# Kernel optimization log

Hardware: AMD Instinct MI355X
Metric: run time of the kernel (lower is better)

Reference implementation:

```python
import jax, jax.numpy as jnp
import numpy as np
from jax import lax

DIM, HEADS, HIDDEN = 384, 6, 1536
B, D, H, W = 2, 14, 14, 14
LN_EPS = 1e-5


def setup_inputs() -> dict:
    key = jax.random.key(0)
    ks = jax.random.split(key, 8)
    s = 0.02
    return {
        "x": jax.random.normal(ks[0], (B, DIM, D, H, W), jnp.float32),
        "conv_w": jax.random.normal(ks[1], (DIM, 1, 3, 3, 3), jnp.float32) * s,
        "conv_b": jnp.zeros((DIM,), jnp.float32),
        "ln1_w": jnp.ones((DIM,), jnp.float32),
        "ln1_b": jnp.zeros((DIM,), jnp.float32),
        "qkv_w": jax.random.normal(ks[2], (3 * DIM, DIM), jnp.float32) * s,
        "proj_w": jax.random.normal(ks[3], (DIM, DIM), jnp.float32) * s,
        "proj_b": jnp.zeros((DIM,), jnp.float32),
        "ln2_w": jnp.ones((DIM,), jnp.float32),
        "ln2_b": jnp.zeros((DIM,), jnp.float32),
        "fc1_w": jax.random.normal(ks[4], (HIDDEN, DIM), jnp.float32) * s,
        "fc1_b": jnp.zeros((HIDDEN,), jnp.float32),
        "fc2_w": jax.random.normal(ks[5], (DIM, HIDDEN), jnp.float32) * s,
        "fc2_b": jnp.zeros((DIM,), jnp.float32),
    }


def _layernorm(x, w, b):
    mu = jnp.mean(x, axis=-1, keepdims=True)
    var = jnp.var(x, axis=-1, keepdims=True)
    return (x - mu) * lax.rsqrt(var + LN_EPS) * w + b


def reference(x, conv_w, conv_b, ln1_w, ln1_b, qkv_w, proj_w, proj_b,
              ln2_w, ln2_b, fc1_w, fc1_b, fc2_w, fc2_b):
    Bn, C = x.shape[0], x.shape[1]
    Dd, Hh, Ww = x.shape[2], x.shape[3], x.shape[4]
    # depthwise conv3d positional embedding (groups=dim), padding=1
    pos = lax.conv_general_dilated(
        x, conv_w, window_strides=(1, 1, 1), padding="SAME",
        feature_group_count=C,
        dimension_numbers=("NCDHW", "OIDHW", "NCDHW"))
    x = x + pos + conv_b[None, :, None, None, None] * 0 + conv_b[None, :, None, None, None]
    # fix: bias belongs to conv output only once
    x = x - conv_b[None, :, None, None, None]
    N = Dd * Hh * Ww
    t = x.reshape(Bn, C, N).transpose(0, 2, 1)  # [B, N, C]

    # attention
    hd = C // HEADS
    scale = hd ** -0.5
    tn = _layernorm(t, ln1_w, ln1_b)
    qkv = tn @ qkv_w.T  # [B, N, 3C]
    qkv = qkv.reshape(Bn, N, 3, HEADS, hd).transpose(2, 0, 3, 1, 4)
    q, k, v = qkv[0], qkv[1], qkv[2]  # [B, H, N, hd]
    attn = jax.nn.softmax(jnp.einsum("bhnd,bhmd->bhnm", q, k) * scale, axis=-1)
    o = jnp.einsum("bhnm,bhmd->bhnd", attn, v)
    o = o.transpose(0, 2, 1, 3).reshape(Bn, N, C)
    t = t + o @ proj_w.T + proj_b

    # MLP (exact GELU, matching torch nn.GELU default)
    tn2 = _layernorm(t, ln2_w, ln2_b)
    h = jax.nn.gelu(tn2 @ fc1_w.T + fc1_b, approximate=False)
    t = t + h @ fc2_w.T + fc2_b

    return t.transpose(0, 2, 1).reshape(Bn, C, Dd, Hh, Ww)
```

## Files before the change

### kernel.cpp

```cpp
#include <hip/hip_runtime.h>
#include <hip/hip_bf16.h>
#include <math.h>

#define DIM 384
#define HEADS 6
#define HIDDEN 1536
#define NTOK 2744
#define NTOKP 2752
#define BATCH 2
#define MTOT (BATCH * NTOK)
#define KSPLIT 4
#define NQT 11
#define CEXP 0.18033688f

typedef __bf16 bf16x8 __attribute__((ext_vector_type(8)));
typedef __bf16 bf16x4 __attribute__((ext_vector_type(4)));
typedef float  f32x4  __attribute__((ext_vector_type(4)));

#define F_GELU  1
#define F_RESID 2
#define F_BF16  4
#define F_QKV   8
#define F_TRANS 16

__device__ __forceinline__ void gll16(const void* g, void* l) {
    __builtin_amdgcn_global_load_lds(
        (const __attribute__((address_space(1))) unsigned int*)g,
        (__attribute__((address_space(3))) unsigned int*)l, 16, 0, 0);
}

__global__ void k_conv(const float* __restrict__ x, const float* __restrict__ cw,
                       float* __restrict__ t,
                       const float* __restrict__ w0, const float* __restrict__ w1,
                       const float* __restrict__ w2, const float* __restrict__ w3,
                       __bf16* o0, __bf16* o1, __bf16* o2, __bf16* o3,
                       __bf16* vt_pad) {
    int bid = blockIdx.x;
    if (bid >= 2256) {
        #pragma unroll
        for (int k = 0; k < 6; k++) {
            int idx = k * 256 + threadIdx.x;
            int row = idx >> 1, half = idx & 1;
            bf16x4 z4 = { (__bf16)0.f, (__bf16)0.f, (__bf16)0.f, (__bf16)0.f };
            *(bf16x4*)(vt_pad + (size_t)row * NTOKP + 2732 + half * 16) = z4;
        }
        return;
    }
    if (bid >= 528) {
        int i = (bid - 528) * 256 + threadIdx.x;
        const float* s; __bf16* d; int off;
        if (i < 110592)      { s = w0; d = o0; off = i; }
        else if (i < 147456) { s = w1; d = o1; off = i - 110592; }
        else if (i < 294912) { s = w2; d = o2; off = i - 147456; }
        else                 { s = w3; d = o3; off = i - 294912; }
        float4 v = ((const float4*)s)[off];
        bf16x4 bb = { (__bf16)v.x, (__bf16)v.y, (__bf16)v.z, (__bf16)v.w };
        *(bf16x4*)(d + (size_t)off * 4) = bb;
        return;
    }
    int nb = bid % 11, rest = bid / 11;
    int cb = rest % 24, b = rest / 24;
    int c0 = cb * 16;
    int n = nb * 256 + threadIdx.x;
    if (n >= NTOK) return;
    int d = n / 196, r = n % 196, h = r / 14, w = r % 14;
    const float* xb = x + ((size_t)b * DIM + c0) * NTOK;
    float acc[16];
    #pragma unroll
    for (int c = 0; c < 16; c++) acc[c] = xb[(size_t)c * NTOK + n];
    #pragma unroll
    for (int kd = 0; kd < 3; kd++) {
        int dd = d + kd - 1;
        if (dd < 0 || dd >= 14) continue;
        #pragma unroll
        for (int kh = 0; kh < 3; kh++) {
            int hh = h + kh - 1;
            if (hh < 0 || hh >= 14) continue;
            #pragma unroll
            for (int kw = 0; kw < 3; kw++) {
                int ww = w + kw - 1;
                if (ww < 0 || ww >= 14) continue;
                int np = (dd * 14 + hh) * 14 + ww;
                int tap = kd * 9 + kh * 3 + kw;
                #pragma unroll
                for (int c = 0; c < 16; c++)
                    acc[c] = fmaf(cw[(c0 + c) * 27 + tap], xb[(size_t)c * NTOK + np], acc[c]);
            }
        }
    }
    float* tp = t + (size_t)(b * NTOK + n) * DIM + c0;
    #pragma unroll
    for (int c = 0; c < 16; c += 4) {
        float4 v = { acc[c], acc[c + 1], acc[c + 2], acc[c + 3] };
        *(float4*)(tp + c) = v;
    }
}

__device__ __forceinline__ void ln_body(const float* __restrict__ in,
                                        __bf16* __restrict__ out,
                                        const float* __restrict__ w,
                                        const float* __restrict__ b) {
    int wid = threadIdx.x >> 6, lane = threadIdx.x & 63;
    int token = blockIdx.x * 4 + wid;
    const float* row = in + (size_t)token * DIM;
    float v[6], s = 0.f, s2 = 0.f;
    #pragma unroll
    for (int i = 0; i < 6; i++) {
        v[i] = row[lane + 64 * i];
        s += v[i]; s2 += v[i] * v[i];
    }
    #pragma unroll
    for (int m = 1; m < 64; m <<= 1) { s += __shfl_xor(s, m); s2 += __shfl_xor(s2, m); }
    float mu = s * (1.f / DIM);
    float rstd = rsqrtf(s2 * (1.f / DIM) - mu * mu + 1e-5f);
    __bf16* orow = out + (size_t)token * DIM;
    #pragma unroll
    for (int i = 0; i < 6; i++) {
        int c = lane + 64 * i;
        orow[c] = (__bf16)((v[i] - mu) * rstd * w[c] + b[c]);
    }
}
__global__ void k_ln1(const float* in, __bf16* out, const float* w, const float* b) {
    ln_body(in, out, w, b);
}
__global__ void k_ln2(const float* in, __bf16* out, const float* w, const float* b) {
    ln_body(in, out, w, b);
}

__device__ __forceinline__ void gemm12864_body(
    const __bf16* __restrict__ A, const __bf16* __restrict__ B,
    const float* __restrict__ bias, void* __restrict__ out,
    __bf16* __restrict__ vt_out, int M, int N, int K, int flags) {
    __shared__ __bf16 As[128][64];
    __shared__ __bf16 Bs[64][64];
    int tid = threadIdx.x, lane = tid & 63, wid = tid >> 6;
    int quad = lane >> 4, l16 = lane & 15;
    int wm = wid & 1, wn = wid >> 1;
    int m0 = blockIdx.y * 128, n0 = blockIdx.x * 64;
    int x7 = l16 & 7;

    auto stage = [&](int k0) {
        #pragma unroll
        for (int i = 0; i < 4; i++) {
            int c = i * 256 + tid;
            int row = c >> 3, cc = (c & 7) ^ (row & 7);
            int gm = m0 + row; if (gm > M - 1) gm = M - 1;
            gll16(A + (size_t)gm * K + k0 + cc * 8, &As[0][0] + (size_t)c * 8);
        }
        #pragma unroll
        for (int i = 0; i < 2; i++) {
            int c = i * 256 + tid;
            int row = c >> 3, cc = (c & 7) ^ (row & 7);
            gll16(B + (size_t)(n0 + row) * K + k0 + cc * 8, &Bs[0][0] + (size_t)c * 8);
        }
    };

    f32x4 acc[4][2] = {};
    int nk = K >> 6;
    for (int ki = 0; ki < nk; ki++) {
        if (ki) __syncthreads();
        stage(ki << 6);
        __syncthreads();
        #pragma unroll
        for (int s = 0; s < 2; s++) {
            bf16x8 a[4], b[2];
            #pragma unroll
            for (int i = 0; i < 4; i++)
                a[i] = *(bf16x8*)&As[wm * 64 + i * 16 + l16][(((s * 4 + quad) ^ x7)) * 8];
            #pragma unroll
            for (int j = 0; j < 2; j++)
                b[j] = *(bf16x8*)&Bs[wn * 32 + j * 16 + l16][(((s * 4 + quad) ^ x7)) * 8];
            #pragma unroll
            for (int i = 0; i < 4; i++)
                #pragma unroll
                for (int j = 0; j < 2; j++)
                    acc[i][j] = __builtin_amdgcn_mfma_f32_16x16x32_bf16(a[i], b[j], acc[i][j], 0, 0, 0);
        }
    }

    int colb = n0 + wn * 32;
    #pragma unroll
    for (int j = 0; j < 2; j++) {
        int col = colb + j * 16 + l16;
        float bv = bias ? bias[col] : 0.f;
        #pragma unroll
        for (int i = 0; i < 4; i++) {
            int row0 = m0 + wm * 64 + i * 16 + quad * 4;
            if (row0 >= M) continue;
            float v4[4];
            #pragma unroll
            for (int r = 0; r < 4; r++) {
                float v = acc[i][j][r] + bv;
                if (flags & F_GELU) v = 0.5f * v * (1.f + erff(v * 0.70710678f));
                if ((flags & F_QKV) && col < 384) v *= CEXP;
                v4[r] = v;
            }
            if ((flags & F_QKV) && col >= 768) {
                int b2 = row0 / NTOK, n2 = row0 - b2 * NTOK;
                int n2p = (n2 & ~63) | (((n2 >> 2) & 3) << 4) | (((n2 >> 4) & 3) << 2);
                bf16x4 pk = { (__bf16)v4[0], (__bf16)v4[1], (__bf16)v4[2], (__bf16)v4[3] };
                *(bf16x4*)(vt_out + ((size_t)(b2 * DIM + (col - 768))) * NTOKP + n2p) = pk;
            } else {
                #pragma unroll
                for (int r = 0; r < 4; r++)
                    ((__bf16*)out)[(size_t)(row0 + r) * N + col] = (__bf16)v4[r];
            }
        }
    }
}
__global__ __launch_bounds__(256) void k_qkv(const __bf16* A, const __bf16* B,
        void* out, __bf16* vt_out, int M, int N, int K) {
    gemm12864_body(A, B, nullptr, out, vt_out, M, N, K, F_QKV);
}
__global__ __launch_bounds__(256) void k_fc1(const __bf16* A, const __bf16* B,
        const float* bias, void* out, int M, int N, int K) {
    gemm12864_body(A, B, bias, out, nullptr, M, N, K, F_GELU | F_BF16);
}

__device__ __forceinline__ void gemm64_body(
    const __bf16* __restrict__ A, const __bf16* __restrict__ B,
    const float* __restrict__ bias, const float* __restrict__ resid,
    void* __restrict__ out, int M, int N, int K, int flags) {
    __shared__ __align__(16) char sm[17408];
    __bf16 (*As)[64] = (__bf16(*)[64])sm;
    __bf16 (*Bs)[64] = (__bf16(*)[64])(sm + 8192);
    float* Tt = (float*)sm;
    int tid = threadIdx.x, lane = tid & 63, wid = tid >> 6;
    int quad = lane >> 4, l16 = lane & 15;
    int wm = wid & 1, wn = wid >> 1;
    int m0 = blockIdx.y * 64, n0 = blockIdx.x * 64;
    int x7 = l16 & 7;

    auto stage = [&](int k0) {
        #pragma unroll
        for (int i = 0; i < 2; i++) {
            int c = i * 256 + tid;
            int row = c >> 3, cc = (c & 7) ^ (row & 7);
            int gm = m0 + row; if (gm > M - 1) gm = M - 1;
            gll16(A + (size_t)gm * K + k0 + cc * 8, &As[0][0] + (size_t)c * 8);
        }
        #pragma unroll
        for (int i = 0; i < 2; i++) {
            int c = i * 256 + tid;
            int row = c >> 3, cc = (c & 7) ^ (row & 7);
            gll16(B + (size_t)(n0 + row) * K + k0 + cc * 8, &Bs[0][0] + (size_t)c * 8);
        }
    };

    f32x4 acc[2][2] = {};
    int nk = K >> 6;
    for (int ki = 0; ki < nk; ki++) {
        if (ki) __syncthreads();
        stage(ki << 6);
        __syncthreads();
        #pragma unroll
        for (int s = 0; s < 2; s++) {
            bf16x8 a[2], b[2];
            #pragma unroll
            for (int i = 0; i < 2; i++)
                a[i] = *(bf16x8*)&As[wm * 32 + i * 16 + l16][(((s * 4 + quad) ^ x7)) * 8];
            #pragma unroll
            for (int j = 0; j < 2; j++)
                b[j] = *(bf16x8*)&Bs[wn * 32 + j * 16 + l16][(((s * 4 + quad) ^ x7)) * 8];
            #pragma unroll
            for (int i = 0; i < 2; i++)
                #pragma unroll
                for (int j = 0; j < 2; j++)
                    acc[i][j] = __builtin_amdgcn_mfma_f32_16x16x32_bf16(a[i], b[j], acc[i][j], 0, 0, 0);
        }
    }

    if (flags & F_TRANS) {
        #pragma unroll
        for (int half = 0; half < 2; half++) {
            __syncthreads();
            if (wn == half) {
                #pragma unroll
                for (int j = 0; j < 2; j++) {
                    int colL = j * 16 + l16;
                    int col = n0 + half * 32 + colL;
                    float bv = bias[col];
                    #pragma unroll
                    for (int i = 0; i < 2; i++) {
                        int rowL = wm * 32 + i * 16 + quad * 4;
                        float v4[4];
                        #pragma unroll
                        for (int r = 0; r < 4; r++) {
                            int rr = m0 + rowL + r; if (rr > M - 1) rr = M - 1;
                            v4[r] = acc[i][j][r] + bv + resid[(size_t)rr * N + col];
                        }
                        float4 pk = { v4[0], v4[1], v4[2], v4[3] };
                        *(float4*)&Tt[colL * 68 + rowL] = pk;
                    }
                }
            }
            __syncthreads();
            int c = tid >> 3, no = (tid & 7) * 8;
            int col = n0 + half * 32 + c;
            #pragma unroll
            for (int q2 = 0; q2 < 2; q2++) {
                int nn = no + q2 * 4;
                int row = m0 + nn;
                if (row >= M) continue;
                int b2 = row / NTOK, n2 = row - b2 * NTOK;
                float4 v = *(float4*)&Tt[c * 68 + nn];
                *(float4*)((float*)out + ((size_t)(b2 * N + col)) * NTOK + n2) = v;
            }
        }
        return;
    }

    #pragma unroll
    for (int j = 0; j < 2; j++) {
        int col = n0 + wn * 32 + j * 16 + l16;
        float bv = bias ? bias[col] : 0.f;
        #pragma unroll
        for (int i = 0; i < 2; i++) {
            int row0 = m0 + wm * 32 + i * 16 + quad * 4;
            if (row0 >= M) continue;
            #pragma unroll
            for (int r = 0; r < 4; r++) {
                float v = acc[i][j][r] + bv;
                if (flags & F_RESID) v += resid[(size_t)(row0 + r) * N + col];
                ((float*)out)[(size_t)(row0 + r) * N + col] = v;
            }
        }
    }
}
__global__ __launch_bounds__(256) void k_proj(const __bf16* A, const __bf16* B,
        const float* bias, const float* resid, void* out, int M, int N, int K) {
    gemm64_body(A, B, bias, resid, out, M, N, K, F_RESID);
}
__global__ __launch_bounds__(256) void k_fc2(const __bf16* A, const __bf16* B,
        const float* bias, const float* resid, void* out, int M, int N, int K) {
    gemm64_body(A, B, bias, resid, out, M, N, K, F_RESID | F_TRANS);
}

__global__ __launch_bounds__(512, 4) void k_attn(const __bf16* __restrict__ qkv,
                                                 const __bf16* __restrict__ vt,
                                                 __bf16* __restrict__ opart,
                                                 float* __restrict__ lpart) {
    __shared__ __align__(16) __bf16 KV[2][2][64][64];
    __bf16 (*Qs)[64] = (__bf16(*)[64])KV;

    int tid = threadIdx.x, lane = tid & 63, wid = tid >> 6;
    int quad = lane >> 4, l16 = lane & 15;
    int flat = blockIdx.x;
    int xcd = flat & 7, slot = flat >> 3;
    int grp = slot / 11, qb = slot - grp * 11;
    int g = xcd + 8 * grp;
    int bh = g % 12, ks = g / 12;
    int q0 = qb * 256;
    int b = bh / HEADS, h = bh % HEADS;
    int x7 = l16 & 7;

    int kt0 = (43 * ks) / KSPLIT, kt1 = (43 * (ks + 1)) / KSPLIT;

    int srow = tid >> 3, scc = (tid & 7) ^ (srow & 7);
    const __bf16* pK = qkv + ((size_t)(b * NTOK + kt0 * 64 + srow)) * 1152 + 384 + h * 64 + scc * 8;
    const __bf16* pV = vt + ((size_t)(bh * 64 + srow)) * NTOKP + kt0 * 64 + scc * 8;

    auto stageKV = [&](int kt, int bufi) {
        const __bf16* kp = pK + (size_t)(kt - kt0) * (64 * 1152);
        if (kt == 42 && srow >= 56)
            kp = qkv + ((size_t)(b * NTOK + NTOK - 1)) * 1152 + 384 + h * 64 + scc * 8;
        gll16(kp, &KV[bufi][0][0][0] + (size_t)tid * 8);
        gll16(pV + (size_t)(kt - kt0) * 64, &KV[bufi][1][0][0] + (size_t)tid * 8);
    };

    #pragma unroll
    for (int i = 0; i < 4; i++) {
        int c = i * 512 + tid;
        int row = c >> 3, cc = (c & 7) ^ (row & 7);
        int gq = q0 + row; if (gq > NTOK - 1) gq = NTOK - 1;
        gll16(qkv + ((size_t)(b * NTOK + gq)) * 1152 + h * 64 + cc * 8,
              &Qs[0][0] + (size_t)c * 8);
    }
    __syncthreads();

    bf16x8 aq[2][2];
    #pragma unroll
    for (int qt = 0; qt < 2; qt++)
        #pragma unroll
        for (int sx = 0; sx < 2; sx++)
            aq[qt][sx] = *(bf16x8*)&Qs[wid * 32 + qt * 16 + l16][((sx * 4 + quad) ^ x7) * 8];
    __syncthreads();

    stageKV(kt0, 0);

    int koff0 = (quad ^ x7) * 8, koff1 = ((4 + quad) ^ x7) * 8;
    int voff0 = ((quad * 2 + 0) ^ x7) * 8, voff1 = ((quad * 2 + 1) ^ x7) * 8;

    const f32x4 fzero = {0.f, 0.f, 0.f, 0.f};
    f32x4 oaccT[2][4] = {};
    float l_sum[2] = {0.f, 0.f};

    int bufi = 0;
    for (int kt = kt0; kt < kt1; kt++) {
        __syncthreads();
        if (kt + 1 < kt1) stageKV(kt + 1, bufi ^ 1);

        const __bf16* ksb = &KV[bufi][0][0][0] + l16 * 64;
        const __bf16* vtb = &KV[bufi][1][0][0] + l16 * 64;
        bool tail = (kt == 42);

        bf16x8 pb[2][2];
        #pragma unroll
        for (int t = 0; t < 4; t++) {
            bf16x8 bk0 = *(bf16x8*)(ksb + t * 1024 + koff0);
            bf16x8 bk1 = *(bf16x8*)(ksb + t * 1024 + koff1);
            #pragma unroll
            for (int qt = 0; qt < 2; qt++) {
                f32x4 z = __builtin_amdgcn_mfma_f32_16x16x32_bf16(bk0, aq[qt][0], fzero, 0, 0, 0);
                z = __builtin_amdgcn_mfma_f32_16x16x32_bf16(bk1, aq[qt][1], z, 0, 0, 0);
                float e0 = exp2f(z[0]), e1 = exp2f(z[1]), e2 = exp2f(z[2]), e3 = exp2f(z[3]);
                if (tail) {
                    int kb = kt * 64 + t * 16 + quad * 4;
                    if (kb + 0 >= NTOK) e0 = 0.f;
                    if (kb + 1 >= NTOK) e1 = 0.f;
                    if (kb + 2 >= NTOK) e2 = 0.f;
                    if (kb + 3 >= NTOK) e3 = 0.f;
                }
                l_sum[qt] += (e0 + e1) + (e2 + e3);
                int half = (t & 1) * 4, px = t >> 1;
                pb[qt][px][half + 0] = (__bf16)e0;
                pb[qt][px][half + 1] = (__bf16)e1;
                pb[qt][px][half + 2] = (__bf16)e2;
                pb[qt][px][half + 3] = (__bf16)e3;
            }
        }

        #pragma unroll
        for (int dt = 0; dt < 4; dt++) {
            const __bf16* vr = vtb + dt * 1024;
            bf16x8 av0 = *(bf16x8*)(vr + voff0);
            bf16x8 av1 = *(bf16x8*)(vr + voff1);
            #pragma unroll
            for (int qt = 0; qt < 2; qt++) {
                oaccT[qt][dt] = __builtin_amdgcn_mfma_f32_16x16x32_bf16(av0, pb[qt][0], oaccT[qt][dt], 0, 0, 0);
                oaccT[qt][dt] = __builtin_amdgcn_mfma_f32_16x16x32_bf16(av1, pb[qt][1], oaccT[qt][dt], 0, 0, 0);
            }
        }
        bufi ^= 1;
    }

    #pragma unroll
    for (int qt = 0; qt < 2; qt++) {
        float l = l_sum[qt];
        l += __shfl_xor(l, 16);
        l += __shfl_xor(l, 32);
        int gq = q0 + wid * 32 + qt * 16 + l16;
        if (quad == 0 && gq < NTOK)
            lpart[((size_t)ks * 12 + bh) * NTOK + gq] = l;
    }

    __bf16* op = opart + ((((size_t)(ks * 12 + bh) * 11 + qb) * 8 + wid) * 2048);
    #pragma unroll
    for (int qt = 0; qt < 2; qt++)
        #pragma unroll
        for (int dt = 0; dt < 4; dt++) {
            bf16x4 pk = { (__bf16)oaccT[qt][dt][0], (__bf16)oaccT[qt][dt][1],
                          (__bf16)oaccT[qt][dt][2], (__bf16)oaccT[qt][dt][3] };
            *(bf16x4*)(op + ((qt * 4 + dt) * 64 + lane) * 4) = pk;
        }
}

__global__ void k_comb(const __bf16* __restrict__ opart,
                       const float* __restrict__ lpart,
                       __bf16* __restrict__ o) {
    int idx = blockIdx.x * 256 + threadIdx.x;
    int token = idx / 96, rem = idx - token * 96;
    int c = rem * 4, h = c >> 6;
    int b2 = token / NTOK, n = token - b2 * NTOK;
    int bh = b2 * HEADS + h;
    int qb = n >> 8, nb = n & 255;
    int wid = nb >> 5, qt = (nb >> 4) & 1, l16 = nb & 15;
    int ch = c & 63, dt = ch >> 4, quad = (ch >> 2) & 3;
    int lane = quad * 16 + l16;
    size_t gbase = ((((size_t)bh * 11 + qb) * 8 + wid) * 512 + (qt * 4 + dt) * 64 + lane) * 4;
    const size_t kstride = (size_t)12 * 11 * 8 * 2048;
    float a0 = 0.f, a1 = 0.f, a2 = 0.f, a3 = 0.f, l = 0.f;
    #pragma unroll
    for (int ks = 0; ks < KSPLIT; ks++) {
        bf16x4 p = *(const bf16x4*)&opart[(size_t)ks * kstride + gbase];
        a0 += (float)p[0]; a1 += (float)p[1]; a2 += (float)p[2]; a3 += (float)p[3];
        l += lpart[((size_t)ks * 12 + bh) * NTOK + n];
    }
    float inv = 1.f / l;
    bf16x4 ov = { (__bf16)(a0 * inv), (__bf16)(a1 * inv),
                  (__bf16)(a2 * inv), (__bf16)(a3 * inv) };
    *(bf16x4*)(o + (size_t)token * DIM + c) = ov;
}

extern "C" void kernel_launch(void* const* d_in, const int* in_sizes, int n_in,
                              void* d_out, int out_size, void* d_ws, size_t ws_size,
                              hipStream_t stream) {
    const float* x      = (const float*)d_in[0];
    const float* conv_w = (const float*)d_in[1];
    const float* ln1_w  = (const float*)d_in[3];
    const float* ln1_b  = (const float*)d_in[4];
    const float* qkv_w  = (const float*)d_in[5];
    const float* proj_w = (const float*)d_in[6];
    const float* proj_b = (const float*)d_in[7];
    const float* ln2_w  = (const float*)d_in[8];
    const float* ln2_b  = (const float*)d_in[9];
    const float* fc1_w  = (const float*)d_in[10];
    const float* fc1_b  = (const float*)d_in[11];
    const float* fc2_w  = (const float*)d_in[12];
    const float* fc2_b  = (const float*)d_in[13];
    float* out = (float*)d_out;

    char* p = (char*)d_ws;
    float*  T    = (float*)p;  p += (size_t)MTOT * DIM * 4;
    __bf16* TN   = (__bf16*)p; p += (size_t)MTOT * DIM * 2;
    __bf16* QKV  = (__bf16*)p; p += (size_t)MTOT * 1152 * 2;
    __bf16* VT   = (__bf16*)p; p += (size_t)BATCH * DIM * NTOKP * 2;
    __bf16* O    = (__bf16*)p; p += (size_t)MTOT * DIM * 2;
    __bf16* H    = (__bf16*)p; p += (size_t)MTOT * HIDDEN * 2;
    __bf16* WQ   = (__bf16*)p; p += (size_t)1152 * 384 * 2;
    __bf16* WP   = (__bf16*)p; p += (size_t)384 * 384 * 2;
    __bf16* W1   = (__bf16*)p; p += (size_t)1536 * 384 * 2;
    __bf16* W2   = (__bf16*)p; p += (size_t)384 * 1536 * 2;
    float*  LP   = (float*)p;  p += (size_t)KSPLIT * 12 * NTOK * 4;
    __bf16* OP   = (__bf16*)p; p += (size_t)KSPLIT * 12 * 11 * 8 * 2048 * 2;

    k_conv<<<528 + 1728 + 1, 256, 0, stream>>>(
        x, conv_w, T, qkv_w, proj_w, fc1_w, fc2_w, WQ, WP, W1, W2, VT);
    k_ln1<<<MTOT / 4, 256, 0, stream>>>(T, TN, ln1_w, ln1_b);
    k_qkv<<<dim3(18, 43), 256, 0, stream>>>(TN, WQ, QKV, VT, MTOT, 1152, 384);
    k_attn<<<528, 512, 0, stream>>>(QKV, VT, OP, LP);
    k_comb<<<(MTOT * 96) / 256, 256, 0, stream>>>(OP, LP, O);
    k_proj<<<dim3(6, 86), 256, 0, stream>>>(O, WP, proj_b, T, T, MTOT, 384, 384);
    k_ln2<<<MTOT / 4, 256, 0, stream>>>(T, TN, ln2_w, ln2_b);
    k_fc1<<<dim3(24, 43), 256, 0, stream>>>(TN, W1, fc1_b, H, MTOT, 1536, 384);
    k_fc2<<<dim3(6, 86), 256, 0, stream>>>(H, W2, fc2_b, T, out, MTOT, 384, 1536);
}
```

Baseline: 236.1 us.

## Drop LDS staging in attention, load K/V fragments directly from global

The attention kernel no longer stages K and V tiles through double-buffered shared memory with barriers. Each wave now loads its MFMA operand fragments straight from global memory (relying on L1/L2 for reuse), and blocks shrink from 512 to 256 threads covering 128 queries, which doubles the grid. The goal is to remove the LDS round trip and the per-iteration __syncthreads. In exchange, each wave issues its own global loads and K/V reuse across the block's waves depends on cache hits, which may raise memory traffic and latency.

Result: slower. 292.4 us (+23.8%).

```diff
diff --git a/kernel.cpp b/kernel.cpp
--- a/kernel.cpp
+++ b/kernel.cpp
@@ -10,7 +10,7 @@
 #define BATCH 2
 #define MTOT (BATCH * NTOK)
 #define KSPLIT 4
-#define NQT 11
+#define NQB 22
 #define CEXP 0.18033688f
 
 typedef __bf16 bf16x8 __attribute__((ext_vector_type(8)));
@@ -336,79 +336,59 @@
     gemm64_body(A, B, bias, resid, out, M, N, K, F_RESID | F_TRANS);
 }
 
-__global__ __launch_bounds__(512, 4) void k_attn(const __bf16* __restrict__ qkv,
+__global__ __launch_bounds__(256, 4) void k_attn(const __bf16* __restrict__ qkv,
                                                  const __bf16* __restrict__ vt,
                                                  __bf16* __restrict__ opart,
                                                  float* __restrict__ lpart) {
-    __shared__ __align__(16) __bf16 KV[2][2][64][64];
-    __bf16 (*Qs)[64] = (__bf16(*)[64])KV;
-
     int tid = threadIdx.x, lane = tid & 63, wid = tid >> 6;
     int quad = lane >> 4, l16 = lane & 15;
     int flat = blockIdx.x;
     int xcd = flat & 7, slot = flat >> 3;
-    int grp = slot / 11, qb = slot - grp * 11;
+    int grp = slot / NQB, qb = slot - grp * NQB;
     int g = xcd + 8 * grp;
     int bh = g % 12, ks = g / 12;
-    int q0 = qb * 256;
     int b = bh / HEADS, h = bh % HEADS;
-    int x7 = l16 & 7;
+    int q0 = qb * 128 + wid * 32;
 
     int kt0 = (43 * ks) / KSPLIT, kt1 = (43 * (ks + 1)) / KSPLIT;
 
-    int srow = tid >> 3, scc = (tid & 7) ^ (srow & 7);
-    const __bf16* pK = qkv + ((size_t)(b * NTOK + kt0 * 64 + srow)) * 1152 + 384 + h * 64 + scc * 8;
-    const __bf16* pV = vt + ((size_t)(bh * 64 + srow)) * NTOKP + kt0 * 64 + scc * 8;
-
-    auto stageKV = [&](int kt, int bufi) {
-        const __bf16* kp = pK + (size_t)(kt - kt0) * (64 * 1152);
-        if (kt == 42 && srow >= 56)
-            kp = qkv + ((size_t)(b * NTOK + NTOK - 1)) * 1152 + 384 + h * 64 + scc * 8;
-        gll16(kp, &KV[bufi][0][0][0] + (size_t)tid * 8);
-        gll16(pV + (size_t)(kt - kt0) * 64, &KV[bufi][1][0][0] + (size_t)tid * 8);
-    };
-
-    #pragma unroll
-    for (int i = 0; i < 4; i++) {
-        int c = i * 512 + tid;
-        int row = c >> 3, cc = (c & 7) ^ (row & 7);
-        int gq = q0 + row; if (gq > NTOK - 1) gq = NTOK - 1;
-        gll16(qkv + ((size_t)(b * NTOK + gq)) * 1152 + h * 64 + cc * 8,
-              &Qs[0][0] + (size_t)c * 8);
-    }
-    __syncthreads();
-
     bf16x8 aq[2][2];
     #pragma unroll
-    for (int qt = 0; qt < 2; qt++)
+    for (int qt = 0; qt < 2; qt++) {
+        int gq = q0 + qt * 16 + l16; if (gq > NTOK - 1) gq = NTOK - 1;
+        const __bf16* qr = qkv + (size_t)(b * NTOK + gq) * 1152 + h * 64;
         #pragma unroll
         for (int sx = 0; sx < 2; sx++)
-            aq[qt][sx] = *(bf16x8*)&Qs[wid * 32 + qt * 16 + l16][((sx * 4 + quad) ^ x7) * 8];
-    __syncthreads();
-
-    stageKV(kt0, 0);
-
-    int koff0 = (quad ^ x7) * 8, koff1 = ((4 + quad) ^ x7) * 8;
-    int voff0 = ((quad * 2 + 0) ^ x7) * 8, voff1 = ((quad * 2 + 1) ^ x7) * 8;
+            aq[qt][sx] = *(const bf16x8*)(qr + (sx * 4 + quad) * 8);
+    }
+
+    const __bf16* kbase[4];
+    const __bf16* vbase[4];
+    #pragma unroll
+    for (int t = 0; t < 4; t++) {
+        kbase[t] = qkv + (size_t)(b * NTOK + kt0 * 64 + t * 16 + l16) * 1152
+                 + 384 + h * 64 + quad * 8;
+        vbase[t] = vt + (size_t)(bh * 64 + t * 16 + l16) * NTOKP
+                 + kt0 * 64 + quad * 16;
+    }
+    const __bf16* kclamp = qkv + (size_t)(b * NTOK + NTOK - 1) * 1152
+                         + 384 + h * 64 + quad * 8;
 
     const f32x4 fzero = {0.f, 0.f, 0.f, 0.f};
     f32x4 oaccT[2][4] = {};
     float l_sum[2] = {0.f, 0.f};
 
-    int bufi = 0;
     for (int kt = kt0; kt < kt1; kt++) {
-        __syncthreads();
-        if (kt + 1 < kt1) stageKV(kt + 1, bufi ^ 1);
-
-        const __bf16* ksb = &KV[bufi][0][0][0] + l16 * 64;
-        const __bf16* vtb = &KV[bufi][1][0][0] + l16 * 64;
         bool tail = (kt == 42);
 
         bf16x8 pb[2][2];
         #pragma unroll
         for (int t = 0; t < 4; t++) {
-            bf16x8 bk0 = *(bf16x8*)(ksb + t * 1024 + koff0);
-            bf16x8 bk1 = *(bf16x8*)(ksb + t * 1024 + koff1);
+            const __bf16* kp = kbase[t];
+            if (tail && (t * 16 + l16 >= 56))
+                kp = kclamp;
+            bf16x8 bk0 = *(const bf16x8*)(kp);
+            bf16x8 bk1 = *(const bf16x8*)(kp + 32);
             #pragma unroll
             for (int qt = 0; qt < 2; qt++) {
                 f32x4 z = __builtin_amdgcn_mfma_f32_16x16x32_bf16(bk0, aq[qt][0], fzero, 0, 0, 0);
@@ -432,16 +412,21 @@
 
         #pragma unroll
         for (int dt = 0; dt < 4; dt++) {
-            const __bf16* vr = vtb + dt * 1024;
-            bf16x8 av0 = *(bf16x8*)(vr + voff0);
-            bf16x8 av1 = *(bf16x8*)(vr + voff1);
+            const __bf16* vp = vbase[dt];
+            bf16x8 av0 = *(const bf16x8*)(vp);
+            bf16x8 av1 = *(const bf16x8*)(vp + 8);
             #pragma unroll
             for (int qt = 0; qt < 2; qt++) {
                 oaccT[qt][dt] = __builtin_amdgcn_mfma_f32_16x16x32_bf16(av0, pb[qt][0], oaccT[qt][dt], 0, 0, 0);
                 oaccT[qt][dt] = __builtin_amdgcn_mfma_f32_16x16x32_bf16(av1, pb[qt][1], oaccT[qt][dt], 0, 0, 0);
             }
         }
-        bufi ^= 1;
+
+        #pragma unroll
+        for (int t = 0; t < 4; t++) {
+            kbase[t] += (size_t)64 * 1152;
+            vbase[t] += 64;
+        }
     }
 
     #pragma unroll
@@ -449,12 +434,12 @@
         float l = l_sum[qt];
         l += __shfl_xor(l, 16);
         l += __shfl_xor(l, 32);
-        int gq = q0 + wid * 32 + qt * 16 + l16;
+        int gq = q0 + qt * 16 + l16;
         if (quad == 0 && gq < NTOK)
             lpart[((size_t)ks * 12 + bh) * NTOK + gq] = l;
     }
 
-    __bf16* op = opart + ((((size_t)(ks * 12 + bh) * 11 + qb) * 8 + wid) * 2048);
+    __bf16* op = opart + (((size_t)(ks * 12 + bh) * NQB + qb) * 4 + wid) * 2048;
     #pragma unroll
     for (int qt = 0; qt < 2; qt++)
         #pragma unroll
@@ -473,12 +458,13 @@
     int c = rem * 4, h = c >> 6;
     int b2 = token / NTOK, n = token - b2 * NTOK;
     int bh = b2 * HEADS + h;
-    int qb = n >> 8, nb = n & 255;
+    int qb = n >> 7, nb = n & 127;
     int wid = nb >> 5, qt = (nb >> 4) & 1, l16 = nb & 15;
     int ch = c & 63, dt = ch >> 4, quad = (ch >> 2) & 3;
     int lane = quad * 16 + l16;
-    size_t gbase = ((((size_t)bh * 11 + qb) * 8 + wid) * 512 + (qt * 4 + dt) * 64 + lane) * 4;
-    const size_t kstride = (size_t)12 * 11 * 8 * 2048;
+    size_t gbase = (((size_t)bh * NQB + qb) * 4 + wid) * 2048
+                 + ((qt * 4 + dt) * 64 + lane) * 4;
+    const size_t kstride = (size_t)12 * NQB * 4 * 2048;
     float a0 = 0.f, a1 = 0.f, a2 = 0.f, a3 = 0.f, l = 0.f;
     #pragma unroll
     for (int ks = 0; ks < KSPLIT; ks++) {
@@ -522,13 +508,13 @@
     __bf16* W1   = (__bf16*)p; p += (size_t)1536 * 384 * 2;
     __bf16* W2   = (__bf16*)p; p += (size_t)384 * 1536 * 2;
     float*  LP   = (float*)p;  p += (size_t)KSPLIT * 12 * NTOK * 4;
-    __bf16* OP   = (__bf16*)p; p += (size_t)KSPLIT * 12 * 11 * 8 * 2048 * 2;
+    __bf16* OP   = (__bf16*)p; p += (size_t)KSPLIT * 12 * NQB * 4 * 2048 * 2;
 
     k_conv<<<528 + 1728 + 1, 256, 0, stream>>>(
         x, conv_w, T, qkv_w, proj_w, fc1_w, fc2_w, WQ, WP, W1, W2, VT);
     k_ln1<<<MTOT / 4, 256, 0, stream>>>(T, TN, ln1_w, ln1_b);
     k_qkv<<<dim3(18, 43), 256, 0, stream>>>(TN, WQ, QKV, VT, MTOT, 1152, 384);
-    k_attn<<<528, 512, 0, stream>>>(QKV, VT, OP, LP);
+    k_attn<<<NQB * 12 * KSPLIT, 256, 0, stream>>>(QKV, VT, OP, LP);
     k_comb<<<(MTOT * 96) / 256, 256, 0, stream>>>(OP, LP, O);
     k_proj<<<dim3(6, 86), 256, 0, stream>>>(O, WP, proj_b, T, T, MTOT, 384, 384);
     k_ln2<<<MTOT / 4, 256, 0, stream>>>(T, TN, ln2_w, ln2_b);
```
